# Optimization experiments

Hardware: AMD Instinct MI355X
Metric: run time of the kernel (lower is better)

The kernel has to match this reference:

```python
import jax, jax.numpy as jnp
import numpy as np

NUM_TOKENS = 4096
IN_FEATURES = 4096
OUT_FEATURES = 4096
MAX_PACKED = 4


def setup_inputs() -> dict:
    key = jax.random.key(0)
    k1, k2, k3 = jax.random.split(key, 3)
    x = jax.random.normal(k1, (NUM_TOKENS, IN_FEATURES), dtype=jnp.float32)
    weight_stacked = jax.random.normal(
        k2, (MAX_PACKED, OUT_FEATURES, IN_FEATURES), dtype=jnp.float32) * 0.02
    indices = jax.random.randint(k3, (NUM_TOKENS,), 0, MAX_PACKED, dtype=jnp.int32)
    return {"x": x, "weight_stacked": weight_stacked, "indices": indices}


def reference(x, weight_stacked, indices):
    # apply_swap: outputs[t] = x[t] @ weight_stacked[indices[t]].T
    # Grouped-GEMM expressed as E dense GEMMs with masked combine
    # (E = max_packed is a small static constant).
    E = weight_stacked.shape[0]
    out = jnp.zeros((x.shape[0], weight_stacked.shape[1]), dtype=x.dtype)
    for e in range(E):
        sel = (indices == e)[:, None].astype(x.dtype)  # [T,1]
        out = out + sel * jnp.einsum('ti,oi->to', x, weight_stacked[e])
    return out
```

## Files before the change

### kernel.cpp

```cpp
#include <hip/hip_runtime.h>

#define T 4096
#define K 4096
#define O 4096
#define E 4
#define BK 64
#define MAXT128 35

typedef __attribute__((ext_vector_type(8))) short bf16x8;
typedef __attribute__((ext_vector_type(4))) float f32x4;

__device__ __forceinline__ unsigned short f2bf(float f) {
  unsigned int u = __float_as_uint(f);
  u += 0x7fffu + ((u >> 16) & 1u);
  return (unsigned short)(u >> 16);
}

__global__ void build_meta(const int* __restrict__ idx, int* __restrict__ perm,
                           int* __restrict__ meta, int4* __restrict__ t256,
                           int4* __restrict__ t128, int4* __restrict__ sched) {
  const int wave = threadIdx.x >> 6;
  const int lane = threadIdx.x & 63;
  __shared__ int s_off[E + 1];
  __shared__ int rtE[20], rtP[20], rtC[20];
  __shared__ int r_sh;
  int total = 0;
  for (int t0 = 0; t0 < T; t0 += 64)
    total += __popcll(__ballot(idx[t0 + lane] == wave));
  if (lane == 0) s_off[wave + 1] = total;
  __syncthreads();
  if (threadIdx.x == 0) {
    s_off[0] = 0;
    for (int e = 0; e < E; e++) s_off[e + 1] += s_off[e];
  }
  __syncthreads();
  int base = s_off[wave];
  const unsigned long long below = (1ull << lane) - 1ull;
  for (int t0 = 0; t0 < T; t0 += 64) {
    int e = idx[t0 + lane];
    unsigned long long m = __ballot(e == wave);
    if (e == wave) perm[base + __popcll(m & below)] = t0 + lane;
    base += __popcll(m);
  }
  if (threadIdx.x == 0) {
    int n = 0;
    for (int e = 0; e < E; e++) {
      int s = s_off[e], c = s_off[e + 1] - s;
      for (int ro = 0; ro < c; ro += 256) {
        rtE[n] = e; rtP[n] = s + ro; rtC[n] = (c - ro) < 256 ? (c - ro) : 256; n++;
      }
    }
    r_sh = n;
    meta[0] = n * 16;
    int n1 = 0;
    for (int e = 0; e < E; e++) {
      int s = s_off[e], c = s_off[e + 1] - s;
      for (int ro = 0; ro < c; ro += 128)
        t128[n1++] = make_int4(e, s + ro, (c - ro) < 128 ? (c - ro) : 128, 0);
    }
    for (; n1 < MAXT128; n1++) t128[n1] = make_int4(-1, 0, 0, 0);
  }
  __syncthreads();
  const int r = r_sh;
  for (int i = threadIdx.x; i < 16 * r; i += 256)
    t256[i] = make_int4(rtE[i >> 4], rtP[i >> 4], rtC[i >> 4], (i & 15) * 256);
  {
    const int b = threadIdx.x;
    const int ru = r - 16;
    const int xcd = b & 7, s = b >> 3;
    const int rt_ = 4 * (xcd >> 1) + (s >> 3);
    const int nt_ = 8 * (xcd & 1) + (s & 7);
    sched[b * 3 + 0] = make_int4(rt_ * 16 + nt_, 0, 16, 0);
    int sgi = 1, u0 = b * ru, u1 = u0 + ru;
    while (u0 < u1) {
      int tI = 256 + (u0 >> 4), q0 = u0 & 15;
      int avail = 16 - q0, want = u1 - u0;
      int take = want < avail ? want : avail;
      sched[b * 3 + sgi] = make_int4(tI, q0, take, 0);
      sgi++; u0 += take;
    }
    for (; sgi < 3; sgi++) sched[b * 3 + sgi] = make_int4(-1, 0, 0, 0);
  }
}

__global__ void zero_rem(const int* __restrict__ meta, const int4* __restrict__ t256,
                         const int* __restrict__ perm, float* __restrict__ out) {
  const int ntiles = meta[0];
  const int tI = 256 + (int)blockIdx.x / 16;
  if (tI >= ntiles) return;
  const int4 td = t256[tI];
  const int rt = (blockIdx.x & 15) * 16 + ((int)threadIdx.x >> 4);
  if (rt >= td.z) return;
  float4* p = (float4*)(out + (size_t)perm[td.y + rt] * O + td.w) + (threadIdx.x & 15) * 4;
  const float4 z = {0.f, 0.f, 0.f, 0.f};
  p[0] = z; p[1] = z; p[2] = z; p[3] = z;
}

__global__ void convert_kernel(const float4* __restrict__ w4, const float* __restrict__ x,
                               const int* __restrict__ perm,
                               ushort4* __restrict__ wb4, ushort4* __restrict__ xg4) {
  const size_t NW4 = (size_t)E * O * K / 4;
  const size_t NX4 = (size_t)T * K / 4;
  const size_t stride = (size_t)gridDim.x * blockDim.x;
  for (size_t i = (size_t)blockIdx.x * blockDim.x + threadIdx.x; i < NW4 + NX4; i += stride) {
    if (i < NW4) {
      float4 v = w4[i];
      wb4[i] = make_ushort4(f2bf(v.x), f2bf(v.y), f2bf(v.z), f2bf(v.w));
    } else {
      size_t j = i - NW4;
      int p = (int)(j >> 10);
      int c = (int)(j & 1023);
      float4 v = *((const float4*)(x + (size_t)perm[p] * K) + c);
      xg4[j] = make_ushort4(f2bf(v.x), f2bf(v.y), f2bf(v.z), f2bf(v.w));
    }
  }
}

__global__ __launch_bounds__(512, 2)
void gemm8p(const unsigned short* __restrict__ xg, const unsigned short* __restrict__ wbb,
            const int* __restrict__ perm, const int4* __restrict__ t256,
            const int4* __restrict__ sched, float* __restrict__ out) {
  __shared__ unsigned short lds[65536];
  const int bid = blockIdx.x;
  const int tid = threadIdx.x;
  const int wid = tid >> 6, lane = tid & 63;
  const int wr = wid >> 2, wc = wid & 3;
  const int kc4 = lane >> 4;
  unsigned short* ldsw = &lds[wid * 512];

#define GLL(gp, lp) __builtin_amdgcn_global_load_lds( \
    (const __attribute__((address_space(1))) void*)(gp), \
    (__attribute__((address_space(3))) void*)(lp), 16, 0, 0)
#define STAGE_A(bo, kh, ko) do { \
    GLL(srcA0 + (ko) + (kh) * 32, ldsw + (bo) + (kh) * 8192); \
    GLL(srcA1 + (ko) + (kh) * 32, ldsw + (bo) + (kh) * 8192 + 4096); \
  } while (0)
#define STAGE_B(bo, kh, ko) do { \
    GLL(srcB0 + (ko) + (kh) * 32, ldsw + (bo) + 16384 + (kh) * 8192); \
    GLL(srcB1 + (ko) + (kh) * 32, ldsw + (bo) + 16384 + (kh) * 8192 + 4096); \
  } while (0)
#define LOADA(dst, bo, ks, mh) do { _Pragma("unroll") \
    for (int mi = 0; mi < 4; ++mi) \
      dst[mi] = *(const bf16x8*)&lds[(bo) + (ks) * 8192 + aoff[mh][mi]]; } while (0)
#define LOADB(dst, bo, ks) do { _Pragma("unroll") \
    for (int ni = 0; ni < 4; ++ni) \
      dst[ni] = *(const bf16x8*)&lds[(bo) + 16384 + (ks) * 8192 + boff[ni]]; } while (0)
#define MFMA16(A, B, mh) do { _Pragma("unroll") \
    for (int mi = 0; mi < 4; ++mi) _Pragma("unroll") \
      for (int ni = 0; ni < 4; ++ni) \
        acc[(mh) * 4 + mi][ni] = __builtin_amdgcn_mfma_f32_16x16x32_bf16( \
            A[mi], B[ni], acc[(mh) * 4 + mi][ni], 0, 0, 0); } while (0)
#define BAR() do { __builtin_amdgcn_s_barrier(); asm volatile("" ::: "memory"); } while (0)
#define VM4() asm volatile("s_waitcnt vmcnt(4)" ::: "memory")
#define VM0() asm volatile("s_waitcnt vmcnt(0)" ::: "memory")
#define PRIO1() __builtin_amdgcn_s_setprio(1)
#define PRIO0() __builtin_amdgcn_s_setprio(0)

#define KTILE(C, X, koe) do { \
    const int ko = (koe); \
    LOADA(afP, C, 0, 0); LOADB(bfP, C, 0); \
    STAGE_A(X, 0, ko); \
    PRIO1(); MFMA16(afP, bfP, 0); PRIO0(); \
    LOADA(afQ, C, 0, 1); \
    STAGE_B(X, 0, ko); \
    PRIO1(); MFMA16(afQ, bfP, 1); PRIO0(); \
    VM4(); BAR(); \
    LOADA(afP, C, 1, 0); LOADB(bfQ, C, 1); \
    STAGE_A(X, 1, ko); \
    PRIO1(); MFMA16(afP, bfQ, 0); PRIO0(); \
    LOADA(afQ, C, 1, 1); \
    STAGE_B(X, 1, ko); \
    PRIO1(); MFMA16(afQ, bfQ, 1); PRIO0(); \
    VM4(); BAR(); \
  } while (0)

  int aoff[2][4], boff[4];
#pragma unroll
  for (int mh = 0; mh < 2; ++mh)
#pragma unroll
    for (int mi = 0; mi < 4; ++mi) {
      int r = wr * 128 + mh * 64 + mi * 16 + (lane & 15);
      aoff[mh][mi] = (((r >> 1) << 3) + (((((r & 1) << 2) | kc4)) ^ ((r >> 1) & 7))) * 8;
    }
#pragma unroll
  for (int ni = 0; ni < 4; ++ni) {
    int r = wc * 64 + ni * 16 + (lane & 15);
    boff[ni] = (((r >> 1) << 3) + (((((r & 1) << 2) | kc4)) ^ ((r >> 1) & 7))) * 8;
  }

  for (int sg = 0; sg < 3; ++sg) {
    const int4 sd = sched[bid * 3 + sg];
    if (sd.x < 0) break;
    const int4 td = t256[sd.x];
    const int e = td.x, p0 = td.y, rc = td.z, n0 = td.w;
    const int kt0 = sd.y << 2;
    const int nt = sd.z << 2;

    const unsigned short *srcA0, *srcA1, *srcB0, *srcB1;
    {
      const unsigned short* wB = wbb + (size_t)e * O * K + (size_t)n0 * K;
      int s0 = tid, s1 = 512 + tid;
      int b0 = s0 >> 3, v0 = (s0 & 7) ^ (b0 & 7);
      int r0 = b0 * 2 + (v0 >> 2), c0 = v0 & 3;
      int b1 = s1 >> 3, v1 = (s1 & 7) ^ (b1 & 7);
      int r1 = b1 * 2 + (v1 >> 2), c1 = v1 & 3;
      int ra0 = r0 < rc ? r0 : rc - 1;
      int ra1 = r1 < rc ? r1 : rc - 1;
      srcA0 = xg + (size_t)(p0 + ra0) * K + c0 * 8;
      srcA1 = xg + (size_t)(p0 + ra1) * K + c1 * 8;
      srcB0 = wB + (size_t)r0 * K + c0 * 8;
      srcB1 = wB + (size_t)r1 * K + c1 * 8;
    }

    f32x4 acc[8][4] = {};
    bf16x8 afP[4], afQ[4], bfP[4], bfQ[4];

    const int kb = kt0 << 6;
    STAGE_A(0, 0, kb); STAGE_B(0, 0, kb);
    STAGE_A(0, 1, kb); STAGE_B(0, 1, kb);
    VM4(); BAR();

    for (int tp = 0; tp < nt; tp += 2) {
      KTILE(0, 32768, ((tp + 1 < nt ? tp + 1 : tp) + kt0) << 6);
      KTILE(32768, 0, ((tp + 2 < nt ? tp + 2 : tp + 1) + kt0) << 6);
    }
    VM0();

    if (sd.z == 16) {
#pragma unroll
      for (int mh = 0; mh < 2; ++mh)
#pragma unroll
        for (int mi = 0; mi < 4; ++mi) {
          const int rbase = wr * 128 + mh * 64 + mi * 16 + (lane >> 4) * 4;
#pragma unroll
          for (int reg = 0; reg < 4; ++reg) {
            const int pr = rbase + reg;
            if (pr < rc) {
              float* orow = out + (size_t)perm[p0 + pr] * O + n0 + wc * 64 + (lane & 15);
#pragma unroll
              for (int ni = 0; ni < 4; ++ni) orow[ni * 16] = acc[mh * 4 + mi][ni][reg];
            }
          }
        }
    } else {
#pragma unroll
      for (int mh = 0; mh < 2; ++mh)
#pragma unroll
        for (int mi = 0; mi < 4; ++mi) {
          const int rbase = wr * 128 + mh * 64 + mi * 16 + (lane >> 4) * 4;
#pragma unroll
          for (int reg = 0; reg < 4; ++reg) {
            const int pr = rbase + reg;
            if (pr < rc) {
              float* orow = out + (size_t)perm[p0 + pr] * O + n0 + wc * 64 + (lane & 15);
#pragma unroll
              for (int ni = 0; ni < 4; ++ni)
                unsafeAtomicAdd(&orow[ni * 16], acc[mh * 4 + mi][ni][reg]);
            }
          }
        }
    }
  }
}

__global__ __launch_bounds__(256)
void gemm_fb(const float* __restrict__ xf, const float* __restrict__ wf,
             const int* __restrict__ perm, const int4* __restrict__ tiles,
             float* __restrict__ out) {
  __shared__ unsigned short lds_a[128 * 64];
  __shared__ unsigned short lds_b[128 * 64];
  const int4 td = tiles[blockIdx.x];
  if (td.x < 0) return;
  const int e = td.x, p0 = td.y, rc = td.z;
  const int n0 = blockIdx.y * 128;
  const int wave = threadIdx.x >> 6, lane = threadIdx.x & 63;
  const int wr = wave >> 1, wc = wave & 1;
  f32x4 acc[4][4] = {};
  const float* wf_base = wf + (size_t)e * O * K + (size_t)n0 * K;
  for (int k0 = 0; k0 < K; k0 += 64) {
    if (k0) __syncthreads();
#pragma unroll
    for (int i = 0; i < 8; i++) {
      int l4 = i * 256 + (int)threadIdx.x;
      int row = l4 >> 4;
      int c4 = (l4 & 15) << 2;
      int ra = row < rc ? row : (rc - 1);
      const float4 va = *(const float4*)(xf + (size_t)perm[p0 + ra] * K + k0 + c4);
      *(ushort4*)&lds_a[row * 64 + c4] = make_ushort4(f2bf(va.x), f2bf(va.y), f2bf(va.z), f2bf(va.w));
      const float4 vb = *(const float4*)(wf_base + (size_t)row * K + k0 + c4);
      *(ushort4*)&lds_b[row * 64 + c4] = make_ushort4(f2bf(vb.x), f2bf(vb.y), f2bf(vb.z), f2bf(vb.w));
    }
    __syncthreads();
#pragma unroll
    for (int ks = 0; ks < 2; ks++) {
      bf16x8 a2[4], b2[4];
#pragma unroll
      for (int mi = 0; mi < 4; mi++)
        a2[mi] = *(const bf16x8*)&lds_a[(wr * 64 + mi * 16 + (lane & 15)) * 64 + ks * 32 + (lane >> 4) * 8];
#pragma unroll
      for (int ni = 0; ni < 4; ni++)
        b2[ni] = *(const bf16x8*)&lds_b[(wc * 64 + ni * 16 + (lane & 15)) * 64 + ks * 32 + (lane >> 4) * 8];
#pragma unroll
      for (int mi = 0; mi < 4; mi++)
#pragma unroll
        for (int ni = 0; ni < 4; ni++)
          acc[mi][ni] = __builtin_amdgcn_mfma_f32_16x16x32_bf16(a2[mi], b2[ni], acc[mi][ni], 0, 0, 0);
    }
  }
#pragma unroll
  for (int mi = 0; mi < 4; mi++) {
    const int rb = wr * 64 + mi * 16 + (lane >> 4) * 4;
#pragma unroll
    for (int reg = 0; reg < 4; reg++) {
      const int rt = rb + reg;
      if (rt < rc) {
        float* orow = out + (size_t)perm[p0 + rt] * O + n0 + wc * 64 + (lane & 15);
#pragma unroll
        for (int ni = 0; ni < 4; ni++) orow[ni * 16] = acc[mi][ni][reg];
      }
    }
  }
}

extern "C" void kernel_launch(void* const* d_in, const int* in_sizes, int n_in,
                              void* d_out, int out_size, void* d_ws, size_t ws_size,
                              hipStream_t stream) {
  const float* x = (const float*)d_in[0];
  const float* w = (const float*)d_in[1];
  const int* idx = (const int*)d_in[2];
  float* out = (float*)d_out;
  char* ws = (char*)d_ws;

  int* perm = (int*)ws;
  int* meta = (int*)(ws + 16384);
  int4* t256 = (int4*)(ws + 16640);
  int4* t128 = (int4*)(ws + 22528);
  int4* sched = (int4*)(ws + 24576);
  unsigned short* xg = (unsigned short*)(ws + 65536);
  unsigned short* wb = xg + (size_t)T * K;
  const size_t need = 65536 + (size_t)T * K * 2 + (size_t)E * O * K * 2;

  build_meta<<<1, 256, 0, stream>>>(idx, perm, meta, t256, t128, sched);
  if (ws_size >= need) {
    zero_rem<<<768, 256, 0, stream>>>(meta, t256, perm, out);
    convert_kernel<<<2048, 256, 0, stream>>>((const float4*)w, x, perm,
                                             (ushort4*)wb, (ushort4*)xg);
    gemm8p<<<256, 512, 0, stream>>>(xg, wb, perm, t256, sched, out);
  } else {
    gemm_fb<<<dim3(MAXT128, 32), 256, 0, stream>>>(x, w, perm, t128, out);
  }
}
```

Before: 272.8 us.

## Fuse weight fp32-to-bf16 conversion into GEMM B-operand staging

Drops the separate pass that converts all expert weights to bf16. The GEMM now loads fp32 weights into registers, packs them to bf16 with v_cvt_pk_bf16_f32, and writes them into swizzled LDS, reorganizing the k-tile pipeline with new wait counts. This removes a large read/write pass over the weights, but the GEMM now reads twice the weight bytes, and it also adds register pressure and VALU work inside the main loop.

```diff
diff --git a/kernel.cpp b/kernel.cpp
--- a/kernel.cpp
+++ b/kernel.cpp
@@ -14,6 +14,15 @@
   unsigned int u = __float_as_uint(f);
   u += 0x7fffu + ((u >> 16) & 1u);
   return (unsigned short)(u >> 16);
+}
+
+__device__ __forceinline__ bf16x8 pack8(float4 a, float4 b) {
+  union { unsigned int u[4]; bf16x8 v; } r;
+  asm("v_cvt_pk_bf16_f32 %0, %1, %2" : "=v"(r.u[0]) : "v"(a.x), "v"(a.y));
+  asm("v_cvt_pk_bf16_f32 %0, %1, %2" : "=v"(r.u[1]) : "v"(a.z), "v"(a.w));
+  asm("v_cvt_pk_bf16_f32 %0, %1, %2" : "=v"(r.u[2]) : "v"(b.x), "v"(b.y));
+  asm("v_cvt_pk_bf16_f32 %0, %1, %2" : "=v"(r.u[3]) : "v"(b.z), "v"(b.w));
+  return r.v;
 }
 
 __global__ void build_meta(const int* __restrict__ idx, int* __restrict__ perm,
@@ -96,28 +105,20 @@
   p[0] = z; p[1] = z; p[2] = z; p[3] = z;
 }
 
-__global__ void convert_kernel(const float4* __restrict__ w4, const float* __restrict__ x,
-                               const int* __restrict__ perm,
-                               ushort4* __restrict__ wb4, ushort4* __restrict__ xg4) {
-  const size_t NW4 = (size_t)E * O * K / 4;
+__global__ void convert_x(const float* __restrict__ x, const int* __restrict__ perm,
+                          ushort4* __restrict__ xg4) {
   const size_t NX4 = (size_t)T * K / 4;
   const size_t stride = (size_t)gridDim.x * blockDim.x;
-  for (size_t i = (size_t)blockIdx.x * blockDim.x + threadIdx.x; i < NW4 + NX4; i += stride) {
-    if (i < NW4) {
-      float4 v = w4[i];
-      wb4[i] = make_ushort4(f2bf(v.x), f2bf(v.y), f2bf(v.z), f2bf(v.w));
-    } else {
-      size_t j = i - NW4;
-      int p = (int)(j >> 10);
-      int c = (int)(j & 1023);
-      float4 v = *((const float4*)(x + (size_t)perm[p] * K) + c);
-      xg4[j] = make_ushort4(f2bf(v.x), f2bf(v.y), f2bf(v.z), f2bf(v.w));
-    }
+  for (size_t i = (size_t)blockIdx.x * blockDim.x + threadIdx.x; i < NX4; i += stride) {
+    int p = (int)(i >> 10);
+    int c = (int)(i & 1023);
+    float4 v = *((const float4*)(x + (size_t)perm[p] * K) + c);
+    xg4[i] = make_ushort4(f2bf(v.x), f2bf(v.y), f2bf(v.z), f2bf(v.w));
   }
 }
 
 __global__ __launch_bounds__(512, 2)
-void gemm8p(const unsigned short* __restrict__ xg, const unsigned short* __restrict__ wbb,
+void gemm8p(const unsigned short* __restrict__ xg, const float* __restrict__ wf,
             const int* __restrict__ perm, const int4* __restrict__ t256,
             const int4* __restrict__ sched, float* __restrict__ out) {
   __shared__ unsigned short lds[65536];
@@ -131,13 +132,18 @@
 #define GLL(gp, lp) __builtin_amdgcn_global_load_lds( \
     (const __attribute__((address_space(1))) void*)(gp), \
     (__attribute__((address_space(3))) void*)(lp), 16, 0, 0)
-#define STAGE_A(bo, kh, ko) do { \
+#define GLLA(bo, kh, ko) do { \
     GLL(srcA0 + (ko) + (kh) * 32, ldsw + (bo) + (kh) * 8192); \
     GLL(srcA1 + (ko) + (kh) * 32, ldsw + (bo) + (kh) * 8192 + 4096); \
   } while (0)
-#define STAGE_B(bo, kh, ko) do { \
-    GLL(srcB0 + (ko) + (kh) * 32, ldsw + (bo) + 16384 + (kh) * 8192); \
-    GLL(srcB1 + (ko) + (kh) * 32, ldsw + (bo) + 16384 + (kh) * 8192 + 4096); \
+#define BLOAD(kh, ko) do { _Pragma("unroll") \
+    for (int s = 0; s < 2; ++s) { \
+      const float* p_ = srcBF + (size_t)(s * 128 + (tid >> 2)) * K + (ko) + (kh) * 32 + (tid & 3) * 8; \
+      bA[s] = *(const float4*)p_; bB[s] = *(const float4*)(p_ + 4); \
+    } } while (0)
+#define BSTORE(bo, kh) do { _Pragma("unroll") \
+    for (int s = 0; s < 2; ++s) \
+      *(bf16x8*)&lds[(bo) + 16384 + (kh) * 8192 + bslot[s] * 8] = pack8(bA[s], bB[s]); \
   } while (0)
 #define LOADA(dst, bo, ks, mh) do { _Pragma("unroll") \
     for (int mi = 0; mi < 4; ++mi) \
@@ -151,6 +157,8 @@
         acc[(mh) * 4 + mi][ni] = __builtin_amdgcn_mfma_f32_16x16x32_bf16( \
             A[mi], B[ni], acc[(mh) * 4 + mi][ni], 0, 0, 0); } while (0)
 #define BAR() do { __builtin_amdgcn_s_barrier(); asm volatile("" ::: "memory"); } while (0)
+#define LGKM0() asm volatile("s_waitcnt lgkmcnt(0)" ::: "memory")
+#define VM6() asm volatile("s_waitcnt vmcnt(6)" ::: "memory")
 #define VM4() asm volatile("s_waitcnt vmcnt(4)" ::: "memory")
 #define VM0() asm volatile("s_waitcnt vmcnt(0)" ::: "memory")
 #define PRIO1() __builtin_amdgcn_s_setprio(1)
@@ -158,20 +166,18 @@
 
 #define KTILE(C, X, koe) do { \
     const int ko = (koe); \
-    LOADA(afP, C, 0, 0); LOADB(bfP, C, 0); \
-    STAGE_A(X, 0, ko); \
-    PRIO1(); MFMA16(afP, bfP, 0); PRIO0(); \
-    LOADA(afQ, C, 0, 1); \
-    STAGE_B(X, 0, ko); \
-    PRIO1(); MFMA16(afQ, bfP, 1); PRIO0(); \
-    VM4(); BAR(); \
-    LOADA(afP, C, 1, 0); LOADB(bfQ, C, 1); \
-    STAGE_A(X, 1, ko); \
-    PRIO1(); MFMA16(afP, bfQ, 0); PRIO0(); \
-    LOADA(afQ, C, 1, 1); \
-    STAGE_B(X, 1, ko); \
-    PRIO1(); MFMA16(afQ, bfQ, 1); PRIO0(); \
-    VM4(); BAR(); \
+     \
+    LOADA(afP, C, 0, 0); LOADB(bfP, C, 0); LOADA(afQ, C, 0, 1); \
+    BSTORE(C, 1); \
+    BLOAD(0, ko); GLLA(X, 0, ko); \
+    PRIO1(); MFMA16(afP, bfP, 0); MFMA16(afQ, bfP, 1); PRIO0(); \
+    VM6(); LGKM0(); BAR(); \
+     \
+    LOADA(afP, C, 1, 0); LOADB(bfQ, C, 1); LOADA(afQ, C, 1, 1); \
+    BSTORE(X, 0); \
+    BLOAD(1, ko); GLLA(X, 1, ko); \
+    PRIO1(); MFMA16(afP, bfQ, 0); MFMA16(afQ, bfQ, 1); PRIO0(); \
+    VM6(); LGKM0(); BAR(); \
   } while (0)
 
   int aoff[2][4], boff[4];
@@ -186,6 +192,12 @@
   for (int ni = 0; ni < 4; ++ni) {
     int r = wc * 64 + ni * 16 + (lane & 15);
     boff[ni] = (((r >> 1) << 3) + (((((r & 1) << 2) | kc4)) ^ ((r >> 1) & 7))) * 8;
+  }
+  int bslot[2];
+#pragma unroll
+  for (int s = 0; s < 2; ++s) {
+    int row = s * 128 + (tid >> 2), c4 = tid & 3;
+    bslot[s] = ((row >> 1) << 3) + (((((row & 1) << 2) | c4)) ^ ((row >> 1) & 7));
   }
 
   for (int sg = 0; sg < 3; ++sg) {
@@ -196,9 +208,8 @@
     const int kt0 = sd.y << 2;
     const int nt = sd.z << 2;
 
-    const unsigned short *srcA0, *srcA1, *srcB0, *srcB1;
+    const unsigned short *srcA0, *srcA1;
     {
-      const unsigned short* wB = wbb + (size_t)e * O * K + (size_t)n0 * K;
       int s0 = tid, s1 = 512 + tid;
       int b0 = s0 >> 3, v0 = (s0 & 7) ^ (b0 & 7);
       int r0 = b0 * 2 + (v0 >> 2), c0 = v0 & 3;
@@ -208,17 +219,19 @@
       int ra1 = r1 < rc ? r1 : rc - 1;
       srcA0 = xg + (size_t)(p0 + ra0) * K + c0 * 8;
       srcA1 = xg + (size_t)(p0 + ra1) * K + c1 * 8;
-      srcB0 = wB + (size_t)r0 * K + c0 * 8;
-      srcB1 = wB + (size_t)r1 * K + c1 * 8;
-    }
+    }
+    const float* srcBF = wf + (size_t)e * O * K + (size_t)n0 * K;
 
     f32x4 acc[8][4] = {};
     bf16x8 afP[4], afQ[4], bfP[4], bfQ[4];
+    float4 bA[2], bB[2];
 
     const int kb = kt0 << 6;
-    STAGE_A(0, 0, kb); STAGE_B(0, 0, kb);
-    STAGE_A(0, 1, kb); STAGE_B(0, 1, kb);
-    VM4(); BAR();
+    BLOAD(0, kb);
+    GLLA(0, 0, kb); GLLA(0, 1, kb);
+    BSTORE(0, 0);
+    BLOAD(1, kb);
+    VM4(); LGKM0(); BAR();
 
     for (int tp = 0; tp < nt; tp += 2) {
       KTILE(0, 32768, ((tp + 1 < nt ? tp + 1 : tp) + kt0) << 6);
@@ -337,15 +350,13 @@
   int4* t128 = (int4*)(ws + 22528);
   int4* sched = (int4*)(ws + 24576);
   unsigned short* xg = (unsigned short*)(ws + 65536);
-  unsigned short* wb = xg + (size_t)T * K;
-  const size_t need = 65536 + (size_t)T * K * 2 + (size_t)E * O * K * 2;
+  const size_t need = 65536 + (size_t)T * K * 2;
 
   build_meta<<<1, 256, 0, stream>>>(idx, perm, meta, t256, t128, sched);
   if (ws_size >= need) {
     zero_rem<<<768, 256, 0, stream>>>(meta, t256, perm, out);
-    convert_kernel<<<2048, 256, 0, stream>>>((const float4*)w, x, perm,
-                                             (ushort4*)wb, (ushort4*)xg);
-    gemm8p<<<256, 512, 0, stream>>>(xg, wb, perm, t256, sched, out);
+    convert_x<<<2048, 256, 0, stream>>>(x, perm, (ushort4*)xg);
+    gemm8p<<<256, 512, 0, stream>>>(xg, w, perm, t256, sched, out);
   } else {
     gemm_fb<<<dim3(MAXT128, 32), 256, 0, stream>>>(x, w, perm, t128, out);
   }
```

Measured after the change: 342.8 us. +25.6%, slower.
